# Optimization experiments

Hardware: AMD Instinct MI355X
Metric: run time of the kernel (lower is better)

## Reference

```python
import jax, jax.numpy as jnp
import numpy as np

MODEL_DIM = 512
STATE_DIM = 1024
ACTION_DIM = 1000
HEADS = 8
DIM_HEAD = MODEL_DIM // 8      # 64
LANDMARKS = MODEL_DIM // 2     # 256
PINV_ITERS = 6
CONV_K = 33                    # lucidrains residual_conv_kernel default
N_TOKENS = 16383               # seq becomes 16384 after cls token (multiple of LANDMARKS)


def layernorm(x, g, b, eps=1e-5):
    mu = jnp.mean(x, axis=-1, keepdims=True)
    var = jnp.var(x, axis=-1, keepdims=True)
    return (x - mu) * jax.lax.rsqrt(var + eps) * g + b


def moore_penrose_pinv(x, iters=PINV_ITERS):
    # x: [b, h, m, m]
    abs_x = jnp.abs(x)
    col = abs_x.sum(-1)
    row = abs_x.sum(-2)
    z = jnp.swapaxes(x, -1, -2) / (jnp.max(col) * jnp.max(row))
    I = jnp.eye(x.shape[-1], dtype=x.dtype)
    for _ in range(iters):
        xz = x @ z
        z = 0.25 * z @ (13 * I - xz @ (15 * I - xz @ (7 * I - xz)))
    return z


def nystrom_attention(x, qkv_W, conv_W, out_W, out_b):
    # x: [b, n, d]; n divisible by LANDMARKS (no padding branch needed)
    b, n, _ = x.shape
    scale = DIM_HEAD ** -0.5
    qkv = x @ qkv_W                                    # [b, n, 3*h*dh]
    q, k, v = jnp.split(qkv, 3, axis=-1)
    to_heads = lambda t: t.reshape(b, n, HEADS, DIM_HEAD).transpose(0, 2, 1, 3)
    q, k, v = to_heads(q), to_heads(k), to_heads(v)    # [b, h, n, dh]
    q = q * scale
    l = n // LANDMARKS
    q_l = q.reshape(b, HEADS, LANDMARKS, l, DIM_HEAD).mean(3)  # [b,h,m,dh]
    k_l = k.reshape(b, HEADS, LANDMARKS, l, DIM_HEAD).mean(3)
    sim1 = jnp.einsum('bhid,bhjd->bhij', q, k_l)       # [b,h,n,m]
    sim2 = jnp.einsum('bhid,bhjd->bhij', q_l, k_l)     # [b,h,m,m]
    sim3 = jnp.einsum('bhid,bhjd->bhij', q_l, k)       # [b,h,m,n]
    a1 = jax.nn.softmax(sim1, axis=-1)
    a2 = jax.nn.softmax(sim2, axis=-1)
    a3 = jax.nn.softmax(sim3, axis=-1)
    a2_inv = moore_penrose_pinv(a2)
    out = (a1 @ a2_inv) @ (a3 @ v)                     # [b,h,n,dh]
    # residual depthwise conv over sequence dim: treat [b,h,n,dh] as NCHW
    pad = CONV_K // 2
    out = out + jax.lax.conv_general_dilated(
        v, conv_W, window_strides=(1, 1), padding=((pad, pad), (0, 0)),
        dimension_numbers=('NCHW', 'OIHW', 'NCHW'), feature_group_count=HEADS)
    out = out.transpose(0, 2, 1, 3).reshape(b, n, HEADS * DIM_HEAD)
    return out @ out_W + out_b


def trans_layer(h, ln_g, ln_b, qkv_W, conv_W, out_W, out_b):
    # h: [n, d]
    x = h[None]
    x = x + nystrom_attention(layernorm(x, ln_g, ln_b), qkv_W, conv_W, out_W, out_b)
    return x[0]


def setup_inputs() -> dict:
    key = jax.random.key(0)
    ks = jax.random.split(key, 12)
    d = MODEL_DIM
    inp = {
        'h': jax.random.normal(ks[0], (N_TOKENS, STATE_DIM), jnp.float32),
        'W1': jax.random.normal(ks[1], (STATE_DIM, d), jnp.float32) * (STATE_DIM ** -0.5),
        'b1': jnp.zeros((d,), jnp.float32),
        'cls': jax.random.normal(ks[2], (1, d), jnp.float32),
        'ln1_g': jnp.ones((d,), jnp.float32), 'ln1_b': jnp.zeros((d,), jnp.float32),
        'qkv1_W': jax.random.normal(ks[3], (d, 3 * d), jnp.float32) * (d ** -0.5),
        'conv1_W': jax.random.normal(ks[4], (HEADS, 1, CONV_K, 1), jnp.float32) * 0.1,
        'out1_W': jax.random.normal(ks[5], (d, d), jnp.float32) * (d ** -0.5),
        'out1_b': jnp.zeros((d,), jnp.float32),
        'ln2_g': jnp.ones((d,), jnp.float32), 'ln2_b': jnp.zeros((d,), jnp.float32),
        'qkv2_W': jax.random.normal(ks[6], (d, 3 * d), jnp.float32) * (d ** -0.5),
        'conv2_W': jax.random.normal(ks[7], (HEADS, 1, CONV_K, 1), jnp.float32) * 0.1,
        'out2_W': jax.random.normal(ks[8], (d, d), jnp.float32) * (d ** -0.5),
        'out2_b': jnp.zeros((d,), jnp.float32),
        'lnf_g': jnp.ones((d,), jnp.float32), 'lnf_b': jnp.zeros((d,), jnp.float32),
        'fc2_W': jax.random.normal(ks[9], (d, ACTION_DIM), jnp.float32) * (d ** -0.5),
        'fc2_b': jnp.zeros((ACTION_DIM,), jnp.float32),
    }
    return inp


def reference(h, W1, b1, cls, ln1_g, ln1_b, qkv1_W, conv1_W, out1_W, out1_b,
              ln2_g, ln2_b, qkv2_W, conv2_W, out2_W, out2_b,
              lnf_g, lnf_b, fc2_W, fc2_b):
    x = jax.nn.relu(h @ W1 + b1)                 # [N, d]
    x = jnp.concatenate([cls, x], axis=0)        # [N+1, d] (16384)
    x = trans_layer(x, ln1_g, ln1_b, qkv1_W, conv1_W, out1_W, out1_b)
    x = trans_layer(x, ln2_g, ln2_b, qkv2_W, conv2_W, out2_W, out2_b)
    x = layernorm(x, lnf_g, lnf_b)[0]            # cls token
    return x @ fc2_W + fc2_b                     # [action_dim]
```

## Files before the change

### kernel.cpp

```cpp
#include <hip/hip_runtime.h>
#include <math.h>

typedef unsigned short u16;
typedef short bf16x8 __attribute__((ext_vector_type(8)));
typedef float f32x4 __attribute__((ext_vector_type(4)));

__device__ __forceinline__ u16 f2b(float x) {
    unsigned u = __builtin_bit_cast(unsigned, x);
    unsigned r = u + 0x7fffu + ((u >> 16) & 1u);
    return (u16)(r >> 16);
}
__device__ __forceinline__ float b2f(u16 v) {
    return __builtin_bit_cast(float, (unsigned)v << 16);
}
__device__ __forceinline__ void gl_lds16(const u16* g, u16* l) {
    __builtin_amdgcn_global_load_lds(
        (const __attribute__((address_space(1))) unsigned int*)g,
        (__attribute__((address_space(3))) unsigned int*)l, 16, 0, 0);
}
__device__ __forceinline__ float wred_sum(float v) {
#pragma unroll
    for (int o = 32; o > 0; o >>= 1) v += __shfl_down(v, o, 64);
    return v;
}
__device__ __forceinline__ float wred_max(float v) {
#pragma unroll
    for (int o = 32; o > 0; o >>= 1) v = fmaxf(v, __shfl_down(v, o, 64));
    return v;
}

struct GP {
    const u16* A; const u16* B; float* C;
    u16* Q; u16* Kb; u16* V;
    const float* bias;
    long sA, sB, sC;
    int K, ldc, tilesN;
};

template <int BM, int BN, int MODE>
__global__ __launch_bounds__(256) void mgemm(GP p) {
    constexpr int FR = BM / 32;
    constexpr int FC = BN / 32;
    constexpr int LA = BM / 64;
    constexpr int LB = BN / 64;
    __shared__ u16 As[2 * BM * 32] __attribute__((aligned(16)));
    __shared__ u16 Bs[2 * BN * 32] __attribute__((aligned(16)));

    int tid = threadIdx.x, lane = tid & 63, wave = tid >> 6;
    int wm = wave >> 1, wn = wave & 1;
    int nwg = gridDim.x, bid = blockIdx.x;
    int q = nwg >> 3, r = nwg & 7;
    int xcd = bid & 7, local = bid >> 3;
    int swz = (xcd < r ? xcd * (q + 1) : r * (q + 1) + (xcd - r) * q) + local;
    int tm = swz / p.tilesN, tn = swz % p.tilesN;
    int batch = blockIdx.y;
    int m0 = tm * BM, n0 = tn * BN;
    const u16* A = p.A + (long)batch * p.sA;
    const u16* B = p.B + (long)batch * p.sB;

    f32x4 acc[FR][FC];
#pragma unroll
    for (int i = 0; i < FR; i++)
#pragma unroll
        for (int j = 0; j < FC; j++) acc[i][j] = (f32x4){0.f, 0.f, 0.f, 0.f};

    int lr = lane & 15;
    int lcb = (lane >> 4) << 3;
    int quad = lane >> 4, cn = lane & 15;

    auto stage = [&](int buf, int k0) {
        u16* Ad = As + buf * (BM * 32);
        u16* Bd = Bs + buf * (BN * 32);
#pragma unroll
        for (int i = 0; i < LA; i++) {
            int chunk = wave * LA + i;
            gl_lds16(A + (long)(m0 + chunk * 16 + lr) * p.K + k0 + lcb,
                     Ad + chunk * 512 + lane * 8);
        }
#pragma unroll
        for (int i = 0; i < LB; i++) {
            int chunk = wave * LB + i;
            gl_lds16(B + (long)(n0 + chunk * 16 + lr) * p.K + k0 + lcb,
                     Bd + chunk * 512 + lane * 8);
        }
    };

    stage(0, 0);
    __syncthreads();
    int cur = 0;
    for (int k0 = 0; k0 < p.K; k0 += 32) {
        if (k0 + 32 < p.K) stage(cur ^ 1, k0 + 32);
        const u16* Asc = As + cur * (BM * 32);
        const u16* Bsc = Bs + cur * (BN * 32);
        bf16x8 af[FR], bfv[FC];
#pragma unroll
        for (int mi = 0; mi < FR; mi++)
            af[mi] = *(const bf16x8*)(Asc + (wm * FR + mi) * 512 + quad * 128 + cn * 8);
#pragma unroll
        for (int ni = 0; ni < FC; ni++)
            bfv[ni] = *(const bf16x8*)(Bsc + (wn * FC + ni) * 512 + quad * 128 + cn * 8);
#pragma unroll
        for (int mi = 0; mi < FR; mi++)
#pragma unroll
            for (int ni = 0; ni < FC; ni++)
                acc[mi][ni] = __builtin_amdgcn_mfma_f32_16x16x32_bf16(
                    af[mi], bfv[ni], acc[mi][ni], 0, 0, 0);
        __syncthreads();
        cur ^= 1;
    }

    if constexpr (MODE == 4) {
#pragma unroll
        for (int mi = 0; mi < FR; mi++) {
#pragma unroll
            for (int ni = 0; ni < FC; ni++) {
#pragma unroll
                for (int r = 0; r < 4; r++) {
                    int row = m0 + (wm * FR + mi) * 16 + quad * 4 + r;
                    int col = n0 + (wn * FC + ni) * 16 + cn;
                    float v = acc[mi][ni][r];
                    int h = col >> 6, d = col & 63;
                    if (col < 512)
                        p.Q[((long)h * 16384 + row) * 64 + d] = f2b(v * 0.125f);
                    else if (col < 1024)
                        p.Kb[((long)(h - 8) * 16384 + row) * 64 + d] = f2b(v);
                    else
                        p.V[((long)(h - 16) * 16384 + row) * 64 + d] = f2b(v);
                }
            }
        }
    } else {
        float* C = p.C + (long)batch * p.sC;
#pragma unroll
        for (int mi = 0; mi < FR; mi++) {
#pragma unroll
            for (int ni = 0; ni < FC; ni++) {
#pragma unroll
                for (int r = 0; r < 4; r++) {
                    int row = m0 + (wm * FR + mi) * 16 + quad * 4 + r;
                    int col = n0 + (wn * FC + ni) * 16 + cn;
                    float v = acc[mi][ni][r];
                    if (MODE == 0) {
                        C[(long)row * p.ldc + col] = v;
                    } else if (MODE == 1) {
                        C[(long)row * p.ldc + col] = fmaxf(v + p.bias[col], 0.f);
                    } else if (MODE == 2) {
                        C[(long)row * p.ldc + col] += v + p.bias[col];
                    }
                }
            }
        }
    }
}

template <int BM, int BN, int MODE>
static void launch_mgemm(hipStream_t st, GP p, int M, int N, int batch) {
    p.tilesN = N / BN;
    dim3 grid((M / BM) * (N / BN), batch);
    mgemm<BM, BN, MODE><<<grid, 256, 0, st>>>(p);
}

__global__ __launch_bounds__(512) void flash_a3v(
    const u16* __restrict__ QLb, const u16* __restrict__ Kb,
    const u16* __restrict__ VT, float* __restrict__ PART) {
    __shared__ u16 QLs[16384] __attribute__((aligned(16)));
    __shared__ u16 Ks[4096] __attribute__((aligned(16)));
    __shared__ u16 Vs[4096] __attribute__((aligned(16)));
    __shared__ u16 Ps[16384] __attribute__((aligned(16)));
    int tid = threadIdx.x, lane = tid & 63, w = tid >> 6;
    int head = blockIdx.y, split = blockIdx.x;
    const u16* QLh = QLb + (long)head * 256 * 64;
    const u16* Kh = Kb + ((long)head * 16384 + split * 512) * 64;
    const u16* Vh = VT + (long)head * 64 * 16384 + split * 512;
    int quad = lane >> 4, cn = lane & 15;
    int lr = lane & 15, lc = (lane >> 4) << 3;

    for (int c = w; c < 32; c += 8) {
        int rc = c >> 1, kc = c & 1;
        gl_lds16(QLh + (long)(rc * 16 + lr) * 64 + kc * 32 + lc, QLs + c * 512 + lane * 8);
    }
    __syncthreads();
    bf16x8 qf[2][2];
#pragma unroll
    for (int mi = 0; mi < 2; mi++)
#pragma unroll
        for (int kc = 0; kc < 2; kc++)
            qf[mi][kc] = *(const bf16x8*)(QLs + ((w * 2 + mi) * 2 + kc) * 512 +
                                          quad * 128 + cn * 8);

    f32x4 Oacc[2][4];
    float m_i[2][4], l_i[2][4];
#pragma unroll
    for (int i = 0; i < 2; i++)
#pragma unroll
        for (int j = 0; j < 4; j++) {
            Oacc[i][j] = (f32x4){0.f, 0.f, 0.f, 0.f};
            m_i[i][j] = -1e30f;
            l_i[i][j] = 0.f;
        }

    for (int t = 0; t < 8; t++) {
        {
            int i = w;
            int rc = i >> 1, kc = i & 1;
            gl_lds16(Kh + (long)(t * 64 + rc * 16 + lr) * 64 + kc * 32 + lc,
                     Ks + i * 512 + lane * 8);
            gl_lds16(Vh + (long)(rc * 16 + lr) * 16384 + t * 64 + kc * 32 + lc,
                     Vs + i * 512 + lane * 8);
        }
        __syncthreads();
        f32x4 s[2][4];
#pragma unroll
        for (int i = 0; i < 2; i++)
#pragma unroll
            for (int j = 0; j < 4; j++) s[i][j] = (f32x4){0.f, 0.f, 0.f, 0.f};
#pragma unroll
        for (int kc = 0; kc < 2; kc++) {
            bf16x8 kf[4];
#pragma unroll
            for (int ni = 0; ni < 4; ni++)
                kf[ni] = *(const bf16x8*)(Ks + (ni * 2 + kc) * 512 + quad * 128 + cn * 8);
#pragma unroll
            for (int mi = 0; mi < 2; mi++)
#pragma unroll
                for (int ni = 0; ni < 4; ni++)
                    s[mi][ni] = __builtin_amdgcn_mfma_f32_16x16x32_bf16(
                        qf[mi][kc], kf[ni], s[mi][ni], 0, 0, 0);
        }
#pragma unroll
        for (int mi = 0; mi < 2; mi++) {
#pragma unroll
            for (int r = 0; r < 4; r++) {
                float mx = fmaxf(fmaxf(s[mi][0][r], s[mi][1][r]),
                                 fmaxf(s[mi][2][r], s[mi][3][r]));
                mx = fmaxf(mx, __shfl_xor(mx, 1));
                mx = fmaxf(mx, __shfl_xor(mx, 2));
                mx = fmaxf(mx, __shfl_xor(mx, 4));
                mx = fmaxf(mx, __shfl_xor(mx, 8));
                float mold = m_i[mi][r];
                float mnew = fmaxf(mold, mx);
                float alpha = __expf(mold - mnew);
                m_i[mi][r] = mnew;
                float sum = 0.f;
#pragma unroll
                for (int ni = 0; ni < 4; ni++) {
                    float e = __expf(s[mi][ni][r] - mnew);
                    sum += e;
                    int col = ni * 16 + cn;
                    Ps[w * 2048 + (mi * 2 + (col >> 5)) * 512 + ((col >> 3) & 3) * 128 +
                       (quad * 4 + r) * 8 + (col & 7)] = f2b(e);
                    Oacc[mi][ni][r] *= alpha;
                }
                sum += __shfl_xor(sum, 1);
                sum += __shfl_xor(sum, 2);
                sum += __shfl_xor(sum, 4);
                sum += __shfl_xor(sum, 8);
                l_i[mi][r] = l_i[mi][r] * alpha + sum;
            }
        }
        __syncthreads();
#pragma unroll
        for (int kc = 0; kc < 2; kc++) {
            bf16x8 vf[4], pf[2];
#pragma unroll
            for (int nd = 0; nd < 4; nd++)
                vf[nd] = *(const bf16x8*)(Vs + (nd * 2 + kc) * 512 + quad * 128 + cn * 8);
#pragma unroll
            for (int mi = 0; mi < 2; mi++)
                pf[mi] = *(const bf16x8*)(Ps + w * 2048 + (mi * 2 + kc) * 512 +
                                          quad * 128 + cn * 8);
#pragma unroll
            for (int mi = 0; mi < 2; mi++)
#pragma unroll
                for (int nd = 0; nd < 4; nd++)
                    Oacc[mi][nd] = __builtin_amdgcn_mfma_f32_16x16x32_bf16(
                        pf[mi], vf[nd], Oacc[mi][nd], 0, 0, 0);
        }
        __syncthreads();
    }
    float* base = PART + ((long)head * 32 + split) * 16896;
#pragma unroll
    for (int mi = 0; mi < 2; mi++) {
#pragma unroll
        for (int r = 0; r < 4; r++) {
            int row = w * 32 + mi * 16 + quad * 4 + r;
            if (cn == 0) {
                base[row] = m_i[mi][r];
                base[256 + row] = l_i[mi][r];
            }
#pragma unroll
            for (int ni = 0; ni < 4; ni++)
                base[512 + row * 64 + ni * 16 + cn] = Oacc[mi][ni][r];
        }
    }
}

__global__ __launch_bounds__(256) void a3v_combine(const float* __restrict__ PART,
                                                   float* __restrict__ O) {
    int head = blockIdx.x, rg = blockIdx.y;
    int t = threadIdx.x;
    int rl = t >> 6, d = t & 63;
    int row = rg * 4 + rl;
    const float* ph = PART + (long)head * 32 * 16896;
    float m = -1e30f;
#pragma unroll 8
    for (int b = 0; b < 32; b++) m = fmaxf(m, ph[b * 16896 + row]);
    float l = 0.f, o = 0.f;
#pragma unroll 8
    for (int b = 0; b < 32; b++) {
        float a = __expf(ph[b * 16896 + row] - m);
        l += a * ph[b * 16896 + 256 + row];
        o += a * ph[b * 16896 + 512 + row * 64 + d];
    }
    O[((long)head * 256 + row) * 64 + d] = o / l;
}

__global__ __launch_bounds__(256) void attn1_fused(
    const u16* __restrict__ Qb, const u16* __restrict__ KLb,
    const u16* __restrict__ W2T, const float* __restrict__ CONV,
    u16* __restrict__ OUTb) {
    __shared__ u16 lds[32768] __attribute__((aligned(16)));
    u16* Qs = lds;
    u16* KLs = lds + 4096;
    u16* Ps = lds;
    u16* W2s = lds + 16384;
    int tid = threadIdx.x, lane = tid & 63, w = tid >> 6;
    int head = blockIdx.y, n0 = blockIdx.x * 64;
    int quad = lane >> 4, cn = lane & 15;
    int lr = lane & 15, lc = (lane >> 4) << 3;
    const u16* Qh = Qb + (long)head * 16384 * 64;
    const u16* KLh = KLb + (long)head * 256 * 64;
    const u16* W2h = W2T + (long)head * 64 * 256;
#pragma unroll
    for (int c = 0; c < 2; c++)
        gl_lds16(Qh + (long)(n0 + w * 16 + lr) * 64 + c * 32 + lc,
                 Qs + c * 2048 + w * 512 + lane * 8);
#pragma unroll
    for (int c = 0; c < 2; c++)
#pragma unroll
        for (int rg = 0; rg < 4; rg++) {
            int chunk = rg * 4 + w;
            gl_lds16(KLh + (long)(chunk * 16 + lr) * 64 + c * 32 + lc,
                     KLs + c * 8192 + chunk * 512 + lane * 8);
        }
    __syncthreads();
    f32x4 acc[16];
#pragma unroll
    for (int i = 0; i < 16; i++) acc[i] = (f32x4){0.f, 0.f, 0.f, 0.f};
#pragma unroll
    for (int c = 0; c < 2; c++) {
        bf16x8 af = *(const bf16x8*)(Qs + c * 2048 + w * 512 + quad * 128 + cn * 8);
#pragma unroll
        for (int ni = 0; ni < 16; ni++) {
            bf16x8 bfv = *(const bf16x8*)(KLs + c * 8192 + ni * 512 + quad * 128 + cn * 8);
            acc[ni] = __builtin_amdgcn_mfma_f32_16x16x32_bf16(af, bfv, acc[ni], 0, 0, 0);
        }
    }
    __syncthreads();
#pragma unroll
    for (int r = 0; r < 4; r++) {
        float mx = -1e30f;
#pragma unroll
        for (int ni = 0; ni < 16; ni++) mx = fmaxf(mx, acc[ni][r]);
        mx = fmaxf(mx, __shfl_xor(mx, 1));
        mx = fmaxf(mx, __shfl_xor(mx, 2));
        mx = fmaxf(mx, __shfl_xor(mx, 4));
        mx = fmaxf(mx, __shfl_xor(mx, 8));
        float e[16];
        float s = 0.f;
#pragma unroll
        for (int ni = 0; ni < 16; ni++) {
            e[ni] = __expf(acc[ni][r] - mx);
            s += e[ni];
        }
        s += __shfl_xor(s, 1);
        s += __shfl_xor(s, 2);
        s += __shfl_xor(s, 4);
        s += __shfl_xor(s, 8);
        float inv = 1.f / s;
        int prow = w * 16 + quad * 4 + r;
#pragma unroll
        for (int ni = 0; ni < 16; ni++) {
            int k = ni * 16 + cn;
            Ps[(k >> 5) * 2048 + ((k >> 3) & 3) * 512 + prow * 8 + (k & 7)] =
                f2b(e[ni] * inv);
        }
    }
#pragma unroll
    for (int c = 0; c < 8; c++)
        gl_lds16(W2h + (long)(w * 16 + lr) * 256 + c * 32 + lc,
                 W2s + c * 2048 + w * 512 + lane * 8);
    __syncthreads();
    f32x4 acc2[4];
#pragma unroll
    for (int i = 0; i < 4; i++) acc2[i] = (f32x4){0.f, 0.f, 0.f, 0.f};
#pragma unroll
    for (int c = 0; c < 8; c++) {
        bf16x8 af = *(const bf16x8*)(Ps + c * 2048 + quad * 512 + (w * 16 + cn) * 8);
#pragma unroll
        for (int ni = 0; ni < 4; ni++) {
            bf16x8 bfv = *(const bf16x8*)(W2s + c * 2048 + ni * 512 + quad * 128 + cn * 8);
            acc2[ni] = __builtin_amdgcn_mfma_f32_16x16x32_bf16(af, bfv, acc2[ni], 0, 0, 0);
        }
    }
#pragma unroll
    for (int ni = 0; ni < 4; ni++)
#pragma unroll
        for (int r = 0; r < 4; r++) {
            int row = n0 + w * 16 + quad * 4 + r;
            long idx = (long)row * 512 + head * 64 + ni * 16 + cn;
            OUTb[idx] = f2b(CONV[idx] + acc2[ni][r]);
        }
}

#define TILE 64
#define KT 16
#define LDP (TILE + 4)
__global__ __launch_bounds__(256) void gemm_kernel(
    const float* __restrict__ A, const float* __restrict__ B, float* __restrict__ C,
    int M, int N, int K, int lda, int ldb, int ldc,
    long sA, long sB, long sC, int tilesN) {
    int tm = blockIdx.x / tilesN, tn = blockIdx.x % tilesN;
    int batch = blockIdx.y;
    A += (long)batch * sA; B += (long)batch * sB; C += (long)batch * sC;
    int row0 = tm * TILE, col0 = tn * TILE;
    __shared__ float As[KT][LDP];
    __shared__ float Bs[KT][LDP];
    int t = threadIdx.x;
    int tx = t & 15, ty = t >> 4;
    float acc[4][4] = {{0.f}};
    int aRow = t >> 2, aK = (t & 3) << 2;
    int bN = t & 63, bK = (t >> 6) << 2;
    for (int k0 = 0; k0 < K; k0 += KT) {
        {
            int r = row0 + aRow;
            float4 av = make_float4(0.f, 0.f, 0.f, 0.f);
            if (r < M) av = *(const float4*)(A + (long)r * lda + k0 + aK);
            As[aK][aRow] = av.x; As[aK + 1][aRow] = av.y;
            As[aK + 2][aRow] = av.z; As[aK + 3][aRow] = av.w;
        }
        {
            const float* bp = B + (long)(k0 + bK) * ldb + col0 + bN;
            bool ok = col0 + bN < N;
#pragma unroll
            for (int j = 0; j < 4; j++) Bs[bK + j][bN] = ok ? bp[(long)j * ldb] : 0.f;
        }
        __syncthreads();
#pragma unroll
        for (int kk = 0; kk < KT; kk++) {
            float4 a = *(const float4*)&As[kk][ty << 2];
            float4 b = *(const float4*)&Bs[kk][tx << 2];
            acc[0][0] += a.x * b.x; acc[0][1] += a.x * b.y; acc[0][2] += a.x * b.z; acc[0][3] += a.x * b.w;
            acc[1][0] += a.y * b.x; acc[1][1] += a.y * b.y; acc[1][2] += a.y * b.z; acc[1][3] += a.y * b.w;
            acc[2][0] += a.z * b.x; acc[2][1] += a.z * b.y; acc[2][2] += a.z * b.z; acc[2][3] += a.z * b.w;
            acc[3][0] += a.w * b.x; acc[3][1] += a.w * b.y; acc[3][2] += a.w * b.z; acc[3][3] += a.w * b.w;
        }
        __syncthreads();
    }
#pragma unroll
    for (int i = 0; i < 4; i++) {
        int row = row0 + (ty << 2) + i;
        if (row >= M) continue;
        float* cp = C + (long)row * ldc + col0 + (tx << 2);
#pragma unroll
        for (int j = 0; j < 4; j++) {
            int col = col0 + (tx << 2) + j;
            if (col >= N) continue;
            cp[j] = acc[i][j];
        }
    }
}
static void gemm32(hipStream_t st, int M, int N, int K,
                   const float* A, int lda, long sA,
                   const float* B, int ldb, long sB,
                   float* C, int ldc, long sC, int batch) {
    int tilesM = (M + TILE - 1) / TILE, tilesN = (N + TILE - 1) / TILE;
    dim3 grid(tilesM * tilesN, batch);
    gemm_kernel<<<grid, 256, 0, st>>>(A, B, C, M, N, K, lda, ldb, ldc, sA, sB, sC, tilesN);
}

__global__ __launch_bounds__(256) void pinv_chain(const float* __restrict__ xz,
                                                  const float* __restrict__ z,
                                                  float* __restrict__ zn,
                                                  u16* __restrict__ znT) {
    int h = blockIdx.y, c0 = blockIdx.x * 8;
    const float* X = xz + (long)h * 65536;
    const float* Z = z + (long)h * 65536;
    __shared__ float ta[256][8];
    __shared__ float tb[256][8];
    int t = threadIdx.x;
    const float4* X4 = (const float4*)(X + t * 256);
    const float4* Z4 = (const float4*)(Z + t * 256);
    float acc[8];
#pragma unroll
    for (int j = 0; j < 8; j++)
        ta[t][j] = ((t == c0 + j) ? 7.f : 0.f) - X[t * 256 + c0 + j];
    __syncthreads();
#pragma unroll
    for (int j = 0; j < 8; j++) acc[j] = 0.f;
    for (int k4 = 0; k4 < 64; k4++) {
        float4 xv = X4[k4];
#pragma unroll
        for (int j = 0; j < 8; j++)
            acc[j] += xv.x * ta[k4 * 4][j] + xv.y * ta[k4 * 4 + 1][j] +
                      xv.z * ta[k4 * 4 + 2][j] + xv.w * ta[k4 * 4 + 3][j];
    }
#pragma unroll
    for (int j = 0; j < 8; j++)
        tb[t][j] = ((t == c0 + j) ? 15.f : 0.f) - acc[j];
    __syncthreads();
#pragma unroll
    for (int j = 0; j < 8; j++) acc[j] = 0.f;
    for (int k4 = 0; k4 < 64; k4++) {
        float4 xv = X4[k4];
#pragma unroll
        for (int j = 0; j < 8; j++)
            acc[j] += xv.x * tb[k4 * 4][j] + xv.y * tb[k4 * 4 + 1][j] +
                      xv.z * tb[k4 * 4 + 2][j] + xv.w * tb[k4 * 4 + 3][j];
    }
    __syncthreads();
#pragma unroll
    for (int j = 0; j < 8; j++)
        ta[t][j] = ((t == c0 + j) ? 13.f : 0.f) - acc[j];
    __syncthreads();
#pragma unroll
    for (int j = 0; j < 8; j++) acc[j] = 0.f;
    for (int k4 = 0; k4 < 64; k4++) {
        float4 zv = Z4[k4];
#pragma unroll
        for (int j = 0; j < 8; j++)
            acc[j] += zv.x * ta[k4 * 4][j] + zv.y * ta[k4 * 4 + 1][j] +
                      zv.z * ta[k4 * 4 + 2][j] + zv.w * ta[k4 * 4 + 3][j];
    }
#pragma unroll
    for (int j = 0; j < 8; j++) {
        float v = 0.25f * acc[j];
        zn[(long)h * 65536 + t * 256 + c0 + j] = v;
        znT[(long)h * 65536 + (c0 + j) * 256 + t] = f2b(v);
    }
}

__global__ __launch_bounds__(256) void layernorm_bf16(
    const float* __restrict__ x, const float* __restrict__ g,
    const float* __restrict__ b, u16* __restrict__ y) {
    __shared__ float sm[4];
    long base = (long)blockIdx.x * 512;
    int t = threadIdx.x;
    float v0 = x[base + t], v1 = x[base + 256 + t];
    float s = wred_sum(v0 + v1);
    if ((t & 63) == 0) sm[t >> 6] = s;
    __syncthreads();
    float mu = (sm[0] + sm[1] + sm[2] + sm[3]) * (1.f / 512.f);
    __syncthreads();
    float d0 = v0 - mu, d1 = v1 - mu;
    float q = wred_sum(d0 * d0 + d1 * d1);
    if ((t & 63) == 0) sm[t >> 6] = q;
    __syncthreads();
    float var = (sm[0] + sm[1] + sm[2] + sm[3]) * (1.f / 512.f);
    float rstd = rsqrtf(var + 1e-5f);
    y[base + t] = f2b(d0 * rstd * g[t] + b[t]);
    y[base + 256 + t] = f2b(d1 * rstd * g[256 + t] + b[256 + t]);
}

__global__ __launch_bounds__(256) void softmax_rows_cs(float* __restrict__ data,
                                                       u16* __restrict__ outb,
                                                       float* __restrict__ colsum) {
    __shared__ float sm[4];
    float* row = data + (long)blockIdx.x * 256;
    u16* rowb = outb + (long)blockIdx.x * 256;
    int h = blockIdx.x >> 8;
    int t = threadIdx.x;
    float v0 = row[t];
    float m = wred_max(v0);
    if ((t & 63) == 0) sm[t >> 6] = m;
    __syncthreads();
    m = fmaxf(fmaxf(sm[0], sm[1]), fmaxf(sm[2], sm[3]));
    __syncthreads();
    float e = __expf(v0 - m);
    float s = wred_sum(e);
    if ((t & 63) == 0) sm[t >> 6] = s;
    __syncthreads();
    s = sm[0] + sm[1] + sm[2] + sm[3];
    float v = e / s;
    row[t] = v;
    rowb[t] = f2b(v);
    atomicAdd(&colsum[h * 256 + t], v);
}

__global__ void cls_copy(const float* __restrict__ cls, float* __restrict__ X) {
    X[threadIdx.x] = cls[threadIdx.x];
}
__global__ void build_hb(const float* __restrict__ h, u16* __restrict__ dst) {
    long idx = (long)blockIdx.x * 256 + threadIdx.x;
    long row = idx >> 10;
    int col = (int)(idx & 1023);
    float v = (row == 0) ? 0.f : h[((row - 1) << 10) + col];
    dst[idx] = f2b(v);
}
__global__ __launch_bounds__(256) void transpose_to_bf16_t(
    const float* __restrict__ src, u16* __restrict__ dst, int R, int C) {
    __shared__ u16 tile[64][65];
    int tilesC = C >> 6;
    int rt = blockIdx.x / tilesC, ct = blockIdx.x % tilesC;
    int t = threadIdx.x, w = t >> 6, lane = t & 63;
    const float* sp = src + (long)(rt * 64) * C + ct * 64;
#pragma unroll
    for (int k = 0; k < 16; k++) {
        int r = w * 16 + k;
        tile[lane][r] = f2b(sp[(long)r * C + lane]);
    }
    __syncthreads();
    u16* dp = dst + (long)(ct * 64) * R + rt * 64;
#pragma unroll
    for (int k = 0; k < 16; k++) {
        int c = w * 16 + k;
        dp[(long)c * R + lane] = tile[c][lane];
    }
}
__global__ __launch_bounds__(256) void transpose_v(const u16* __restrict__ Vb,
                                                   u16* __restrict__ VT) {
    __shared__ u16 tile[64][68];
    int h = blockIdx.y, n0 = blockIdx.x * 64;
    int t = threadIdx.x;
    int i = t >> 2, seg = t & 3;
    const u16* src = Vb + ((long)h * 16384 + n0 + i) * 64 + seg * 16;
#pragma unroll
    for (int j = 0; j < 16; j++) tile[seg * 16 + j][i] = src[j];
    __syncthreads();
    u16* dst = VT + ((long)h * 64 + i) * 16384 + n0 + seg * 16;
#pragma unroll
    for (int j = 0; j < 16; j++) dst[j] = tile[i][seg * 16 + j];
}
__global__ void landmarks_b(const u16* __restrict__ Qb, const u16* __restrict__ Kb,
                            u16* __restrict__ QLb, u16* __restrict__ KLb) {
    int h = blockIdx.x >> 8, j = blockIdx.x & 255, d = threadIdx.x;
    const u16* qb = Qb + ((long)h * 16384 + j * 64) * 64 + d;
    const u16* kb = Kb + ((long)h * 16384 + j * 64) * 64 + d;
    float sq = 0.f, sk = 0.f;
    for (int tk = 0; tk < 64; ++tk) {
        sq += b2f(qb[tk * 64]);
        sk += b2f(kb[tk * 64]);
    }
    QLb[((h << 8) + j) * 64 + d] = f2b(sq * (1.f / 64.f));
    KLb[((h << 8) + j) * 64 + d] = f2b(sk * (1.f / 64.f));
}

__global__ __launch_bounds__(256) void pinv_absmax_fin(const float* __restrict__ colsum,
                                                       float* __restrict__ maxes) {
    __shared__ float sm[4];
    int t = threadIdx.x;
    float m = 0.f;
#pragma unroll
    for (int h = 0; h < 8; h++) m = fmaxf(m, colsum[h * 256 + t]);
    m = wred_max(m);
    if ((t & 63) == 0) sm[t >> 6] = m;
    __syncthreads();
    if (t == 0) {
        maxes[0] = 1.0f;
        maxes[1] = fmaxf(fmaxf(sm[0], sm[1]), fmaxf(sm[2], sm[3]));
    }
}

__global__ void pinv_init(const float* __restrict__ a2, const float* __restrict__ maxes,
                          float* __restrict__ z, u16* __restrict__ zT) {
    long idx = (long)blockIdx.x * 256 + threadIdx.x;
    int h = (int)(idx >> 16);
    int rem = (int)(idx & 65535);
    int i = rem >> 8, j = rem & 255;
    float inv = 1.f / (maxes[0] * maxes[1]);
    float v = a2[((long)h << 16) + (j << 8) + i] * inv;
    z[idx] = v;
    zT[((long)h << 16) + (j << 8) + i] = f2b(v);
}
__global__ __launch_bounds__(256) void conv_kernel(const u16* __restrict__ VT,
                                                   const float* __restrict__ cw,
                                                   float* __restrict__ out) {
    int h = blockIdx.y;
    int n0 = blockIdx.x * 64;
    __shared__ float vt[64][97];
    int t = threadIdx.x;
    for (int i = t; i < 64 * 96; i += 256) {
        int d = i / 96, j = i % 96;
        int n = n0 - 16 + j;
        float v = 0.f;
        if (n >= 0 && n < 16384) v = b2f(VT[((long)h * 64 + d) * 16384 + n]);
        vt[d][j] = v;
    }
    __syncthreads();
    float w[33];
#pragma unroll
    for (int k = 0; k < 33; k++) w[k] = cw[h * 33 + k];
    int d = t & 63, ty = t >> 6;
    for (int nn = 0; nn < 16; nn++) {
        int nl = ty * 16 + nn;
        float s = 0.f;
#pragma unroll
        for (int k = 0; k < 33; k++) s += w[k] * vt[d][nl + k];
        out[((long)(n0 + nl)) * 512 + h * 64 + d] = s;
    }
}
__global__ void w2t_kernel(const float* __restrict__ W2, u16* __restrict__ W2T) {
    int idx = blockIdx.x * 256 + threadIdx.x;
    int h = idx >> 14, rem = idx & 16383, m = rem >> 6, d = rem & 63;
    W2T[(h << 14) + (d << 8) + m] = f2b(W2[idx]);
}
__global__ __launch_bounds__(256) void final_head(
    const float* __restrict__ X, const float* __restrict__ g, const float* __restrict__ b,
    const float* __restrict__ W, const float* __restrict__ bias, float* __restrict__ out) {
    __shared__ float sm[4];
    __shared__ float ln0[512];
    int t = threadIdx.x;
    float v0 = X[t], v1 = X[256 + t];
    float s = wred_sum(v0 + v1);
    if ((t & 63) == 0) sm[t >> 6] = s;
    __syncthreads();
    float mu = (sm[0] + sm[1] + sm[2] + sm[3]) * (1.f / 512.f);
    __syncthreads();
    float d0 = v0 - mu, d1 = v1 - mu;
    float q = wred_sum(d0 * d0 + d1 * d1);
    if ((t & 63) == 0) sm[t >> 6] = q;
    __syncthreads();
    float rstd = rsqrtf((sm[0] + sm[1] + sm[2] + sm[3]) * (1.f / 512.f) + 1e-5f);
    ln0[t] = d0 * rstd * g[t] + b[t];
    ln0[256 + t] = d1 * rstd * g[256 + t] + b[256 + t];
    __syncthreads();
    int jj = blockIdx.x * 256 + t;
    if (jj < 1000) {
        float acc = bias[jj];
        for (int dd = 0; dd < 512; ++dd) acc += ln0[dd] * W[dd * 1000 + jj];
        out[jj] = acc;
    }
}

struct Bufs {
    float *X, *LNA, *A2, *Z0, *Z1, *XZ, *O, *W2, *MAXES, *COLSUM, *PART;
    u16 *LNb, *Qb, *Kb, *Vb, *VT, *QLb, *KLb, *W2T, *W1T, *QKVWT, *OUTWT;
    u16 *A2b, *ZT0, *ZT1;
};

static void run_layer(hipStream_t st, Bufs& B,
                      const float* ln_g, const float* ln_b, const float* qkv_W,
                      const float* conv_W, const float* out_W, const float* out_b) {
    const int N = 16384, D = 512, H = 8, DH = 64, M = 256;
    GP p{};
    layernorm_bf16<<<N, 256, 0, st>>>(B.X, ln_g, ln_b, B.LNb);
    transpose_to_bf16_t<<<(512 / 64) * (1536 / 64), 256, 0, st>>>(qkv_W, B.QKVWT, 512, 1536);
    p = GP{}; p.A = B.LNb; p.B = B.QKVWT; p.Q = B.Qb; p.Kb = B.Kb; p.V = B.Vb; p.K = 512;
    launch_mgemm<128, 128, 4>(st, p, N, 1536, 1);
    transpose_v<<<dim3(256, 8), 256, 0, st>>>(B.Vb, B.VT);
    landmarks_b<<<H * M, 64, 0, st>>>(B.Qb, B.Kb, B.QLb, B.KLb);
    p = GP{}; p.A = B.QLb; p.B = B.KLb; p.C = B.A2; p.K = DH; p.ldc = M;
    p.sA = (long)M * DH; p.sB = (long)M * DH; p.sC = (long)M * M;
    launch_mgemm<64, 64, 0>(st, p, M, M, H);
    hipMemsetAsync(B.COLSUM, 0, 8 * 256 * 4, st);
    softmax_rows_cs<<<H * M, 256, 0, st>>>(B.A2, B.A2b, B.COLSUM);
    pinv_absmax_fin<<<1, 256, 0, st>>>(B.COLSUM, B.MAXES);
    pinv_init<<<(H * M * M) / 256, 256, 0, st>>>(B.A2, B.MAXES, B.Z0, B.ZT0);
    float* z = B.Z0; float* zn = B.Z1;
    u16* zt = B.ZT0; u16* ztn = B.ZT1;
    for (int it = 0; it < 6; ++it) {
        p = GP{}; p.A = B.A2b; p.B = zt; p.C = B.XZ; p.K = M; p.ldc = M;
        p.sA = (long)M * M; p.sB = (long)M * M; p.sC = (long)M * M;
        launch_mgemm<64, 64, 0>(st, p, M, M, H);
        pinv_chain<<<dim3(32, 8), 256, 0, st>>>(B.XZ, z, zn, ztn);
        float* t1 = z; z = zn; zn = t1;
        u16* t2 = zt; zt = ztn; ztn = t2;
    }
    conv_kernel<<<dim3(N / 64, H), 256, 0, st>>>(B.VT, conv_W, B.LNA);
    flash_a3v<<<dim3(32, 8), 512, 0, st>>>(B.QLb, B.Kb, B.VT, B.PART);
    a3v_combine<<<dim3(8, 64), 256, 0, st>>>(B.PART, B.O);
    gemm32(st, M, DH, M, z, M, (long)M * M, B.O, DH, (long)M * DH,
           B.W2, DH, (long)M * DH, H);
    w2t_kernel<<<512, 256, 0, st>>>(B.W2, B.W2T);
    attn1_fused<<<dim3(N / 64, H), 256, 0, st>>>(B.Qb, B.KLb, B.W2T, B.LNA, B.LNb);
    transpose_to_bf16_t<<<(512 / 64) * (512 / 64), 256, 0, st>>>(out_W, B.OUTWT, 512, 512);
    p = GP{}; p.A = B.LNb; p.B = B.OUTWT; p.C = B.X; p.bias = out_b; p.K = D; p.ldc = D;
    launch_mgemm<128, 128, 2>(st, p, N, D, 1);
}

extern "C" void kernel_launch(void* const* d_in, const int* in_sizes, int n_in,
                              void* d_out, int out_size, void* d_ws, size_t ws_size,
                              hipStream_t stream) {
    const float* h_in = (const float*)d_in[0];
    const float* W1 = (const float*)d_in[1];
    const float* b1 = (const float*)d_in[2];
    const float* cls = (const float*)d_in[3];
    const float* ln1_g = (const float*)d_in[4];
    const float* ln1_b = (const float*)d_in[5];
    const float* qkv1_W = (const float*)d_in[6];
    const float* conv1_W = (const float*)d_in[7];
    const float* out1_W = (const float*)d_in[8];
    const float* out1_b = (const float*)d_in[9];
    const float* ln2_g = (const float*)d_in[10];
    const float* ln2_b = (const float*)d_in[11];
    const float* qkv2_W = (const float*)d_in[12];
    const float* conv2_W = (const float*)d_in[13];
    const float* out2_W = (const float*)d_in[14];
    const float* out2_b = (const float*)d_in[15];
    const float* lnf_g = (const float*)d_in[16];
    const float* lnf_b = (const float*)d_in[17];
    const float* fc2_W = (const float*)d_in[18];
    const float* fc2_b = (const float*)d_in[19];
    float* out = (float*)d_out;

    char* wsb = (char*)d_ws;
    size_t off = 0;
    auto alloc = [&](size_t bytes) -> void* {
        void* p = (void*)(wsb + off);
        off += (bytes + 255) & ~(size_t)255;
        return p;
    };
    Bufs B;
    B.X    = (float*)alloc((size_t)16384 * 512 * 4);
    B.LNA  = (float*)alloc((size_t)16384 * 512 * 4);
    B.LNb  = (u16*)alloc((size_t)16384 * 512 * 2);
    B.Qb   = (u16*)alloc((size_t)8 * 16384 * 64 * 2);
    B.Kb   = (u16*)alloc((size_t)8 * 16384 * 64 * 2);
    B.VT   = (u16*)alloc((size_t)8 * 64 * 16384 * 2);
    B.QLb  = (u16*)alloc((size_t)8 * 256 * 64 * 2);
    B.KLb  = (u16*)alloc((size_t)8 * 256 * 64 * 2);
    B.A2   = (float*)alloc((size_t)8 * 256 * 256 * 4);
    B.A2b  = (u16*)alloc((size_t)8 * 256 * 256 * 2);
    B.Z0   = (float*)alloc((size_t)8 * 256 * 256 * 4);
    B.Z1   = (float*)alloc((size_t)8 * 256 * 256 * 4);
    B.ZT0  = (u16*)alloc((size_t)8 * 256 * 256 * 2);
    B.ZT1  = (u16*)alloc((size_t)8 * 256 * 256 * 2);
    B.XZ   = (float*)alloc((size_t)8 * 256 * 256 * 4);
    B.O    = (float*)alloc((size_t)8 * 256 * 64 * 4);
    B.W2   = (float*)alloc((size_t)8 * 256 * 64 * 4);
    B.W2T  = (u16*)alloc((size_t)8 * 64 * 256 * 2);
    B.W1T  = (u16*)alloc((size_t)512 * 1024 * 2);
    B.QKVWT = (u16*)alloc((size_t)1536 * 512 * 2);
    B.OUTWT = (u16*)alloc((size_t)512 * 512 * 2);
    B.MAXES = (float*)alloc(256);
    B.COLSUM = (float*)alloc((size_t)8 * 256 * 4);
    {
        size_t vb = (size_t)8 * 16384 * 64 * 2;
        size_t part = (size_t)8 * 32 * 16896 * 4;
        void* region = alloc(part > vb ? part : vb);
        B.Vb = (u16*)region;
        B.PART = (float*)region;
    }
    if (off > ws_size) return;

    u16* HB = B.Qb;
    build_hb<<<(16384 * 1024) / 256, 256, 0, stream>>>(h_in, HB);
    transpose_to_bf16_t<<<(1024 / 64) * (512 / 64), 256, 0, stream>>>(W1, B.W1T, 1024, 512);
    {
        GP p{}; p.A = HB; p.B = B.W1T; p.C = B.X; p.bias = b1; p.K = 1024; p.ldc = 512;
        launch_mgemm<128, 128, 1>(stream, p, 16384, 512, 1);
    }
    cls_copy<<<1, 512, 0, stream>>>(cls, B.X);

    run_layer(stream, B, ln1_g, ln1_b, qkv1_W, conv1_W, out1_W, out1_b);
    run_layer(stream, B, ln2_g, ln2_b, qkv2_W, conv2_W, out2_W, out2_b);

    final_head<<<4, 256, 0, stream>>>(B.X, lnf_g, lnf_b, fc2_W, fc2_b, out);
}
```

Measured before the change: 1.282 ms.

## Fuse residual depthwise conv into attention kernel and transpose W2 in gemm epilogue

Computes the 33-tap depthwise conv on V directly inside attn1_fused from a staged LDS tile instead of a separate kernel writing an fp32 buffer. The small fp32 gemm now writes its result transposed in bf16, removing the w2t kernel and the W2 buffer. This removes two launches and a large intermediate round trip through memory, at the cost of extra LDS per block and extra per-thread conv work in the epilogue.

```diff
diff --git a/kernel.cpp b/kernel.cpp
--- a/kernel.cpp
+++ b/kernel.cpp
@@ -317,9 +317,11 @@
 
 __global__ __launch_bounds__(256) void attn1_fused(
     const u16* __restrict__ Qb, const u16* __restrict__ KLb,
-    const u16* __restrict__ W2T, const float* __restrict__ CONV,
-    u16* __restrict__ OUTb) {
+    const u16* __restrict__ W2T, const u16* __restrict__ VT,
+    const float* __restrict__ cw, u16* __restrict__ OUTb) {
     __shared__ u16 lds[32768] __attribute__((aligned(16)));
+    __shared__ u16 vtb[64 * 96] __attribute__((aligned(16)));
+    __shared__ float sw[33];
     u16* Qs = lds;
     u16* KLs = lds + 4096;
     u16* Ps = lds;
@@ -331,6 +333,14 @@
     const u16* Qh = Qb + (long)head * 16384 * 64;
     const u16* KLh = KLb + (long)head * 256 * 64;
     const u16* W2h = W2T + (long)head * 64 * 256;
+    for (int i = tid; i < 64 * 96; i += 256) {
+        int d = i / 96, j = i % 96;
+        int n = n0 - 16 + j;
+        u16 v = 0;
+        if (n >= 0 && n < 16384) v = VT[((long)head * 64 + d) * 16384 + n];
+        vtb[i] = v;
+    }
+    if (tid < 33) sw[tid] = cw[head * 33 + tid];
 #pragma unroll
     for (int c = 0; c < 2; c++)
         gl_lds16(Qh + (long)(n0 + w * 16 + lr) * 64 + c * 32 + lc,
@@ -408,21 +418,26 @@
 #pragma unroll
         for (int r = 0; r < 4; r++) {
             int row = n0 + w * 16 + quad * 4 + r;
-            long idx = (long)row * 512 + head * 64 + ni * 16 + cn;
-            OUTb[idx] = f2b(CONV[idx] + acc2[ni][r]);
+            int dl = ni * 16 + cn;
+            int jb = w * 16 + quad * 4 + r;
+            float cv = 0.f;
+#pragma unroll
+            for (int k = 0; k < 33; k++) cv += sw[k] * b2f(vtb[dl * 96 + jb + k]);
+            long idx = (long)row * 512 + head * 64 + dl;
+            OUTb[idx] = f2b(cv + acc2[ni][r]);
         }
 }
 
 #define TILE 64
 #define KT 16
 #define LDP (TILE + 4)
-__global__ __launch_bounds__(256) void gemm_kernel(
-    const float* __restrict__ A, const float* __restrict__ B, float* __restrict__ C,
-    int M, int N, int K, int lda, int ldb, int ldc,
-    long sA, long sB, long sC, int tilesN) {
+__global__ __launch_bounds__(256) void gemm32t_kernel(
+    const float* __restrict__ A, const float* __restrict__ B, u16* __restrict__ CT,
+    int M, int N, int K, int lda, int ldb,
+    long sA, long sB, int tilesN) {
     int tm = blockIdx.x / tilesN, tn = blockIdx.x % tilesN;
     int batch = blockIdx.y;
-    A += (long)batch * sA; B += (long)batch * sB; C += (long)batch * sC;
+    A += (long)batch * sA; B += (long)batch * sB;
     int row0 = tm * TILE, col0 = tn * TILE;
     __shared__ float As[KT][LDP];
     __shared__ float Bs[KT][LDP];
@@ -461,22 +476,21 @@
     for (int i = 0; i < 4; i++) {
         int row = row0 + (ty << 2) + i;
         if (row >= M) continue;
-        float* cp = C + (long)row * ldc + col0 + (tx << 2);
 #pragma unroll
         for (int j = 0; j < 4; j++) {
             int col = col0 + (tx << 2) + j;
             if (col >= N) continue;
-            cp[j] = acc[i][j];
-        }
-    }
-}
-static void gemm32(hipStream_t st, int M, int N, int K,
-                   const float* A, int lda, long sA,
-                   const float* B, int ldb, long sB,
-                   float* C, int ldc, long sC, int batch) {
+            CT[(long)batch * M * N + (long)col * M + row] = f2b(acc[i][j]);
+        }
+    }
+}
+static void gemm32t(hipStream_t st, int M, int N, int K,
+                    const float* A, int lda, long sA,
+                    const float* B, int ldb, long sB,
+                    u16* CT, int batch) {
     int tilesM = (M + TILE - 1) / TILE, tilesN = (N + TILE - 1) / TILE;
     dim3 grid(tilesM * tilesN, batch);
-    gemm_kernel<<<grid, 256, 0, st>>>(A, B, C, M, N, K, lda, ldb, ldc, sA, sB, sC, tilesN);
+    gemm32t_kernel<<<grid, 256, 0, st>>>(A, B, CT, M, N, K, lda, ldb, sA, sB, tilesN);
 }
 
 __global__ __launch_bounds__(256) void pinv_chain(const float* __restrict__ xz,
@@ -672,38 +686,6 @@
     z[idx] = v;
     zT[((long)h << 16) + (j << 8) + i] = f2b(v);
 }
-__global__ __launch_bounds__(256) void conv_kernel(const u16* __restrict__ VT,
-                                                   const float* __restrict__ cw,
-                                                   float* __restrict__ out) {
-    int h = blockIdx.y;
-    int n0 = blockIdx.x * 64;
-    __shared__ float vt[64][97];
-    int t = threadIdx.x;
-    for (int i = t; i < 64 * 96; i += 256) {
-        int d = i / 96, j = i % 96;
-        int n = n0 - 16 + j;
-        float v = 0.f;
-        if (n >= 0 && n < 16384) v = b2f(VT[((long)h * 64 + d) * 16384 + n]);
-        vt[d][j] = v;
-    }
-    __syncthreads();
-    float w[33];
-#pragma unroll
-    for (int k = 0; k < 33; k++) w[k] = cw[h * 33 + k];
-    int d = t & 63, ty = t >> 6;
-    for (int nn = 0; nn < 16; nn++) {
-        int nl = ty * 16 + nn;
-        float s = 0.f;
-#pragma unroll
-        for (int k = 0; k < 33; k++) s += w[k] * vt[d][nl + k];
-        out[((long)(n0 + nl)) * 512 + h * 64 + d] = s;
-    }
-}
-__global__ void w2t_kernel(const float* __restrict__ W2, u16* __restrict__ W2T) {
-    int idx = blockIdx.x * 256 + threadIdx.x;
-    int h = idx >> 14, rem = idx & 16383, m = rem >> 6, d = rem & 63;
-    W2T[(h << 14) + (d << 8) + m] = f2b(W2[idx]);
-}
 __global__ __launch_bounds__(256) void final_head(
     const float* __restrict__ X, const float* __restrict__ g, const float* __restrict__ b,
     const float* __restrict__ W, const float* __restrict__ bias, float* __restrict__ out) {
@@ -733,7 +715,7 @@
 }
 
 struct Bufs {
-    float *X, *LNA, *A2, *Z0, *Z1, *XZ, *O, *W2, *MAXES, *COLSUM, *PART;
+    float *X, *A2, *Z0, *Z1, *XZ, *O, *MAXES, *COLSUM, *PART;
     u16 *LNb, *Qb, *Kb, *Vb, *VT, *QLb, *KLb, *W2T, *W1T, *QKVWT, *OUTWT;
     u16 *A2b, *ZT0, *ZT1;
 };
@@ -766,13 +748,10 @@
         float* t1 = z; z = zn; zn = t1;
         u16* t2 = zt; zt = ztn; ztn = t2;
     }
-    conv_kernel<<<dim3(N / 64, H), 256, 0, st>>>(B.VT, conv_W, B.LNA);
     flash_a3v<<<dim3(32, 8), 512, 0, st>>>(B.QLb, B.Kb, B.VT, B.PART);
     a3v_combine<<<dim3(8, 64), 256, 0, st>>>(B.PART, B.O);
-    gemm32(st, M, DH, M, z, M, (long)M * M, B.O, DH, (long)M * DH,
-           B.W2, DH, (long)M * DH, H);
-    w2t_kernel<<<512, 256, 0, st>>>(B.W2, B.W2T);
-    attn1_fused<<<dim3(N / 64, H), 256, 0, st>>>(B.Qb, B.KLb, B.W2T, B.LNA, B.LNb);
+    gemm32t(st, M, DH, M, z, M, (long)M * M, B.O, DH, (long)M * DH, B.W2T, H);
+    attn1_fused<<<dim3(N / 64, H), 256, 0, st>>>(B.Qb, B.KLb, B.W2T, B.VT, conv_W, B.LNb);
     transpose_to_bf16_t<<<(512 / 64) * (512 / 64), 256, 0, st>>>(out_W, B.OUTWT, 512, 512);
     p = GP{}; p.A = B.LNb; p.B = B.OUTWT; p.C = B.X; p.bias = out_b; p.K = D; p.ldc = D;
     launch_mgemm<128, 128, 2>(st, p, N, D, 1);
@@ -812,7 +791,6 @@
     };
     Bufs B;
     B.X    = (float*)alloc((size_t)16384 * 512 * 4);
-    B.LNA  = (float*)alloc((size_t)16384 * 512 * 4);
     B.LNb  = (u16*)alloc((size_t)16384 * 512 * 2);
     B.Qb   = (u16*)alloc((size_t)8 * 16384 * 64 * 2);
     B.Kb   = (u16*)alloc((size_t)8 * 16384 * 64 * 2);
@@ -827,7 +805,6 @@
     B.ZT1  = (u16*)alloc((size_t)8 * 256 * 256 * 2);
     B.XZ   = (float*)alloc((size_t)8 * 256 * 256 * 4);
     B.O    = (float*)alloc((size_t)8 * 256 * 64 * 4);
-    B.W2   = (float*)alloc((size_t)8 * 256 * 64 * 4);
     B.W2T  = (u16*)alloc((size_t)8 * 64 * 256 * 2);
     B.W1T  = (u16*)alloc((size_t)512 * 1024 * 2);
     B.QKVWT = (u16*)alloc((size_t)1536 * 512 * 2);
```

After: 1.511 ms. 1.18x slower.
